# Kernel tuning notes

Hardware: AMD Instinct MI355X
Metric: run time of the kernel (lower is better)

## Reference

```python
import jax, jax.numpy as jnp
import numpy as np

N, E, IN, HID, H, L, G = 20000, 320000, 128, 64, 4, 3, 128

def setup_inputs() -> dict:
    key = jax.random.key(0)
    ks = jax.random.split(key, 14)
    x = jax.random.normal(ks[0], (N, IN), dtype=jnp.float32)
    edge_index = jax.random.randint(ks[1], (2, E), 0, N, dtype=jnp.int64)
    batch = jnp.sort(jax.random.randint(ks[2], (N,), 0, G, dtype=jnp.int64))
    s_in = 1.0 / np.sqrt(IN)
    s_h = 1.0 / np.sqrt(HID)
    lin_W = jax.random.normal(ks[3], (IN, HID), jnp.float32) * s_in
    lin_b = jax.random.normal(ks[4], (HID,), jnp.float32) * 0.02
    Wq = jax.random.normal(ks[5], (L, HID, H * HID), jnp.float32) * s_h
    bq = jax.random.normal(ks[6], (L, H * HID), jnp.float32) * 0.02
    Wk = jax.random.normal(ks[7], (L, HID, H * HID), jnp.float32) * s_h
    bk = jax.random.normal(ks[8], (L, H * HID), jnp.float32) * 0.02
    Wv = jax.random.normal(ks[9], (L, HID, H * HID), jnp.float32) * s_h
    bv = jax.random.normal(ks[10], (L, H * HID), jnp.float32) * 0.02
    Ws = jax.random.normal(ks[11], (L, HID, HID), jnp.float32) * s_h
    bs = jax.random.normal(ks[12], (L, HID), jnp.float32) * 0.02
    return {"x": x, "edge_index": edge_index, "batch": batch,
            "lin_W": lin_W, "lin_b": lin_b, "Wq": Wq, "bq": bq,
            "Wk": Wk, "bk": bk, "Wv": Wv, "bv": bv, "Ws": Ws, "bs": bs}

def _transformer_conv(h, src, dst, Wq, bq, Wk, bk, Wv, bv, Ws, bs):
    # PyG TransformerConv(hid, hid, heads=H, concat=False), beta=False, root_weight=True
    n = h.shape[0]
    C = HID  # per-head dim
    q = (h @ Wq + bq).reshape(n, H, C)
    k = (h @ Wk + bk).reshape(n, H, C)
    v = (h @ Wv + bv).reshape(n, H, C)
    # per-edge attention logits: q_i . k_j / sqrt(C), i=dst (target), j=src
    alpha = jnp.einsum('ehc,ehc->eh', q[dst], k[src]) * (1.0 / np.sqrt(C))  # [E,H]
    # segment softmax over edges grouped by target node
    amax = jax.ops.segment_max(alpha, dst, num_segments=n)  # [N,H]
    amax = jnp.where(jnp.isfinite(amax), amax, 0.0)
    ex = jnp.exp(alpha - amax[dst])
    denom = jax.ops.segment_sum(ex, dst, num_segments=n)
    a = ex / jnp.maximum(denom[dst], 1e-16)  # [E,H]
    msg = a[:, :, None] * v[src]  # [E,H,C]
    agg = jax.ops.segment_sum(msg.reshape(-1, H * C), dst, num_segments=n)
    out = agg.reshape(n, H, C).mean(axis=1)  # concat=False -> head mean
    return out + h @ Ws + bs  # root/skip connection

def reference(x, edge_index, batch, lin_W, lin_b, Wq, bq, Wk, bk, Wv, bv, Ws, bs):
    src, dst = edge_index[0], edge_index[1]
    h = x @ lin_W + lin_b  # [N, HID]; dropout inactive in eval
    for l in range(L):
        h = jax.nn.relu(_transformer_conv(h, src, dst, Wq[l], bq[l], Wk[l], bk[l],
                                          Wv[l], bv[l], Ws[l], bs[l]))
    # global_add_pool: sum node features per graph
    return jax.ops.segment_sum(h, batch, num_segments=G)  # [G, HID]
```

## Files before the change

kernel.cpp:

```cpp
#include <hip/hip_runtime.h>
#include <math.h>

#define N_NODES 20000
#define N_EDGES 320000
#define DIM_IN 128
#define HID 64
#define HEADS 4
#define LAYERS 3
#define GRAPHS 128
#define HOP 68

typedef unsigned short ushort;
typedef ushort ushort8 __attribute__((ext_vector_type(8)));
typedef ushort ushort4v __attribute__((ext_vector_type(4)));
typedef short short8 __attribute__((ext_vector_type(8)));
typedef float f32x4 __attribute__((ext_vector_type(4)));

__device__ __forceinline__ float bf2f(ushort u) {
    return __uint_as_float(((unsigned int)u) << 16);
}
__device__ __forceinline__ ushort f2bf(float f) {
    unsigned int b = __float_as_uint(f);
    return (ushort)((b + 0x7FFFu + ((b >> 16) & 1u)) >> 16);
}


__global__ __launch_bounds__(256) void histwcvt_kernel(
        const int* __restrict__ dst, int* __restrict__ counts,
        const float* __restrict__ Wq, const float* __restrict__ bq,
        const float* __restrict__ Wk, const float* __restrict__ bk,
        const float* __restrict__ Wv, const float* __restrict__ bv,
        const float* __restrict__ Ws, const float* __restrict__ bs,
        const float* __restrict__ linW,
        ushort* __restrict__ Wt3, float* __restrict__ bias3,
        ushort* __restrict__ Wlt) {
    const int PER = 832 * 64;
    int idx = blockIdx.x * 256 + threadIdx.x;
    if (idx < N_EDGES) atomicAdd(&counts[dst[idx]], 1);
    if (idx < 3 * PER) {
        int l = idx / PER;
        int r = idx - l * PER;
        int j = r >> 6, k = r & 63;
        const float* Wq_l = Wq + (size_t)l * HID * 256;
        const float* Wk_l = Wk + (size_t)l * HID * 256;
        const float* Wv_l = Wv + (size_t)l * HID * 256;
        const float* Ws_l = Ws + (size_t)l * HID * 64;
        float w;
        if (j < 256) {
            w = Wq_l[(size_t)k * 256 + j];
        } else if (j < 768) {
            int pout = j - 256;
            int isv = (pout >> 2) & 1;
            int low2 = pout & 3;
            int g = pout >> 3;
            int srccol = (g >> 4) * 64 + (g & 15) * 4 + low2;
            w = isv ? Wv_l[(size_t)k * 256 + srccol] : Wk_l[(size_t)k * 256 + srccol];
        } else {
            w = Ws_l[(size_t)k * 64 + (j - 768)];
        }
        Wt3[idx] = f2bf(w);
    } else if (idx < 3 * PER + 64 * DIM_IN) {
        int idx2 = idx - 3 * PER;
        int col = idx2 >> 7, k = idx2 & 127;
        Wlt[idx2] = f2bf(linW[(size_t)k * HID + col]);
    }
    if (idx < 3 * 832) {
        int l = idx / 832, j = idx - l * 832;
        float b;
        if (j < 256) {
            b = bq[l * 256 + j];
        } else if (j < 768) {
            int pout = j - 256;
            int isv = (pout >> 2) & 1;
            int low2 = pout & 3;
            int g = pout >> 3;
            int srccol = (g >> 4) * 64 + (g & 15) * 4 + low2;
            b = isv ? bv[l * 256 + srccol] : bk[l * 256 + srccol];
        } else {
            b = bs[l * 64 + (j - 768)];
        }
        bias3[idx] = b;
    }
}


__global__ __launch_bounds__(256) void blocksum_sortcnt_kernel(const int* __restrict__ counts,
        int* __restrict__ bsum, int* __restrict__ degcnt, int* __restrict__ rankbuf) {
    int i = blockIdx.x * 256 + threadIdx.x;
    int v = (i < N_NODES) ? counts[i] : 0;
    if (i < N_NODES) {
        int key = 1023 - (v < 1023 ? v : 1023);
        rankbuf[i] = atomicAdd(&degcnt[key], 1);
    }
    int lane = threadIdx.x & 63, wave = threadIdx.x >> 6;
    int s = v;
#pragma unroll
    for (int off = 32; off >= 1; off >>= 1) s += __shfl_xor(s, off);
    __shared__ int ws[4];
    if (lane == 0) ws[wave] = s;
    __syncthreads();
    if (threadIdx.x == 0) bsum[blockIdx.x] = ws[0] + ws[1] + ws[2] + ws[3];
}


__global__ __launch_bounds__(1024) void scans_kernel(const int* __restrict__ degcnt,
        int* __restrict__ degoff, const int* __restrict__ bsum, int* __restrict__ bexcl,
        int nb) {
    int tid = threadIdx.x;
    int v = degcnt[tid];
    int lane = tid & 63, wv = tid >> 6;
    int s = v;
#pragma unroll
    for (int off = 1; off < 64; off <<= 1) {
        int t = __shfl_up(s, off);
        if (lane >= off) s += t;
    }
    __shared__ int wsum[16];
    if (lane == 63) wsum[wv] = s;
    __syncthreads();
    int add = 0;
    for (int q = 0; q < wv; ++q) add += wsum[q];
    degoff[tid] = add + s - v;
    if (tid < 64) {
        int v0 = (tid < nb) ? bsum[tid] : 0;
        int s0 = v0;
#pragma unroll
        for (int off = 1; off < 64; off <<= 1) {
            int t = __shfl_up(s0, off);
            if (lane >= off) s0 += t;
        }
        int carry = __shfl(s0, 63);
        int v1 = (tid + 64 < nb) ? bsum[tid + 64] : 0;
        int s1 = v1;
#pragma unroll
        for (int off = 1; off < 64; off <<= 1) {
            int t = __shfl_up(s1, off);
            if (lane >= off) s1 += t;
        }
        if (tid < nb) bexcl[tid] = s0 - v0;
        if (tid + 64 < nb) bexcl[tid + 64] = carry + s1 - v1;
    }
}


__global__ __launch_bounds__(256) void expand_sortscat_kernel(const int* __restrict__ counts,
        const int* __restrict__ bexcl, int* __restrict__ offs, int* __restrict__ cursor,
        const int* __restrict__ degoff, const int* __restrict__ rankbuf,
        int* __restrict__ perm) {
    int i = blockIdx.x * 256 + threadIdx.x;
    int v = (i < N_NODES) ? counts[i] : 0;
    int lane = threadIdx.x & 63, wave = threadIdx.x >> 6;
    int s = v;
#pragma unroll
    for (int off = 1; off < 64; off <<= 1) {
        int t = __shfl_up(s, off);
        if (lane >= off) s += t;
    }
    __shared__ int wsum[4];
    if (lane == 63) wsum[wave] = s;
    __syncthreads();
    int add = bexcl[blockIdx.x];
    for (int w = 0; w < wave; ++w) add += wsum[w];
    int excl = add + s - v;
    if (i < N_NODES) {
        offs[i] = excl;
        cursor[i] = excl;
        int key = 1023 - (v < 1023 ? v : 1023);
        perm[degoff[key] + rankbuf[i]] = i;
    }
    if (i == 0) offs[N_NODES] = N_EDGES;
}

__global__ void scatter_kernel(const int* __restrict__ src, const int* __restrict__ dst,
                               int* __restrict__ cursor, int* __restrict__ csr, int n) {
    int e = blockIdx.x * 256 + threadIdx.x;
    if (e < n) {
        int d = dst[e];
        int pos = atomicAdd(&cursor[d], 1);
        csr[pos] = src[e];
    }
}


__device__ __forceinline__ void proj_rows(const float* __restrict__ ho,
        const ushort* __restrict__ Wt, const float* __restrict__ bias_cat,
        ushort* __restrict__ qsb, ushort* __restrict__ kvp,
        int grow, bool ok, int lane, int t0, int tstep) {
    int lr = lane & 15;
    int koff = (lane >> 4) * 8;
    short8 bh[2];
#pragma unroll
    for (int mm = 0; mm < 2; ++mm) {
        const float* hp = ho + lr * HOP + mm * 32 + koff;
        float4 f0 = *(const float4*)hp;
        float4 f1 = *(const float4*)(hp + 4);
        ushort8 u;
        u[0] = f2bf(f0.x); u[1] = f2bf(f0.y); u[2] = f2bf(f0.z); u[3] = f2bf(f0.w);
        u[4] = f2bf(f1.x); u[5] = f2bf(f1.y); u[6] = f2bf(f1.z); u[7] = f2bf(f1.w);
        bh[mm] = __builtin_bit_cast(short8, u);
    }
    for (int t = t0; t < 52; t += tstep) {
        const ushort* wb = Wt + (size_t)(t * 16 + lr) * HID + koff;
        short8 w0 = *(const short8*)wb;
        short8 w1 = *(const short8*)(wb + 32);
        f32x4 a_ = (f32x4){0.f, 0.f, 0.f, 0.f};
        a_ = __builtin_amdgcn_mfma_f32_16x16x32_bf16(w0, bh[0], a_, 0, 0, 0);
        a_ = __builtin_amdgcn_mfma_f32_16x16x32_bf16(w1, bh[1], a_, 0, 0, 0);
        int j = t * 16 + ((lane >> 4) << 2);
        float4 bs4 = *(const float4*)(bias_cat + j);
        ushort4v u4;
        u4[0] = f2bf(a_[0] + bs4.x);
        u4[1] = f2bf(a_[1] + bs4.y);
        u4[2] = f2bf(a_[2] + bs4.z);
        u4[3] = f2bf(a_[3] + bs4.w);
        if (ok) {
            ushort* dst;
            if (j < 256)      dst = qsb + (size_t)grow * 320 + j;
            else if (j < 768) dst = kvp + (size_t)grow * 512 + (j - 256);
            else              dst = qsb + (size_t)grow * 320 + 256 + (j - 768);
            *(ushort4v*)dst = u4;
        }
    }
}


__global__ __launch_bounds__(256) void linproj_kernel(const float* __restrict__ x,
        const ushort* __restrict__ Wlt, const float* __restrict__ lb,
        const ushort* __restrict__ Wt0, const float* __restrict__ bias0,
        ushort* __restrict__ qsb, ushort* __restrict__ kvp) {
    __shared__ float ho[64 * HOP];
    int tid = threadIdx.x;
    int w = tid >> 6, l = tid & 63;
    int r0 = blockIdx.x * 64 + w * 16;
    int row = r0 + (l & 15);
    int rowc = (row < N_NODES) ? row : (N_NODES - 1);

    short8 a[4];
#pragma unroll
    for (int kc = 0; kc < 4; ++kc) {
        const float* xp = x + (size_t)rowc * DIM_IN + kc * 32 + (l >> 4) * 8;
        float4 f0 = *(const float4*)xp;
        float4 f1 = *(const float4*)(xp + 4);
        ushort8 u;
        u[0] = f2bf(f0.x); u[1] = f2bf(f0.y); u[2] = f2bf(f0.z); u[3] = f2bf(f0.w);
        u[4] = f2bf(f1.x); u[5] = f2bf(f1.y); u[6] = f2bf(f1.z); u[7] = f2bf(f1.w);
        a[kc] = __builtin_bit_cast(short8, u);
    }

    f32x4 acc[4];
#pragma unroll
    for (int t = 0; t < 4; ++t) acc[t] = (f32x4){0.f, 0.f, 0.f, 0.f};

    const ushort* wb = Wlt + (size_t)(l & 15) * DIM_IN + (l >> 4) * 8;
#pragma unroll
    for (int t = 0; t < 4; ++t) {
#pragma unroll
        for (int kc = 0; kc < 4; ++kc) {
            short8 b = *(const short8*)(wb + (size_t)t * 16 * DIM_IN + kc * 32);
            acc[t] = __builtin_amdgcn_mfma_f32_16x16x32_bf16(b, a[kc], acc[t], 0, 0, 0);
        }
    }

    float* hrow = ho + (size_t)(w * 16 + (l & 15)) * HOP;
#pragma unroll
    for (int t = 0; t < 4; ++t) {
        int j = t * 16 + ((l >> 4) << 2);
        float4 bias = *(const float4*)(lb + j);
        float4 o;
        o.x = acc[t][0] + bias.x;
        o.y = acc[t][1] + bias.y;
        o.z = acc[t][2] + bias.z;
        o.w = acc[t][3] + bias.w;
        *(float4*)(hrow + j) = o;
    }
    proj_rows(ho + (size_t)w * 16 * HOP, Wt0, bias0, qsb, kvp,
              row, row < N_NODES, l, 0, 1);
}


__device__ __forceinline__ float4 attn_node(int node, int lane,
        const ushort* __restrict__ qsb, const ushort8* __restrict__ kvp,
        const int* __restrict__ offs, const int* __restrict__ csr) {
    int hh = lane >> 4;
    int cb = (lane & 15) * 4;
    const ushort* nb = qsb + (size_t)node * 320;
    ushort4v qu = *(const ushort4v*)(nb + hh * 64 + cb);
    float qx = bf2f(qu[0]), qy = bf2f(qu[1]), qz = bf2f(qu[2]), qw = bf2f(qu[3]);

    const float SCL = 0.125f * 1.44269504088896340736f;
    float m = -INFINITY, l = 0.f;
    float4 acc = make_float4(0.f, 0.f, 0.f, 0.f);

    int e0 = offs[node], e1 = offs[node + 1];
    int cnt = e1 - e0;

    ushort8 cur = (ushort8)(0);
    ushort8 nxt = (ushort8)(0);
    if (cnt > 0) cur = kvp[(size_t)csr[e0] * 64 + lane];
    if (cnt > 1) nxt = kvp[(size_t)csr[e0 + 1] * 64 + lane];

    for (int i = 0; i < cnt; ++i) {
        ushort8 u = cur;
        cur = nxt;
        if (i + 2 < cnt) nxt = kvp[(size_t)csr[e0 + i + 2] * 64 + lane];

        float p = qx * bf2f(u[0]) + qy * bf2f(u[1]) + qz * bf2f(u[2]) + qw * bf2f(u[3]);
        p += __shfl_xor(p, 1);
        p += __shfl_xor(p, 2);
        p += __shfl_xor(p, 4);
        p += __shfl_xor(p, 8);
        float alpha = p * SCL;
        if (__any(alpha > m)) {
            float nm = fmaxf(m, alpha);
            float sc = exp2f(m - nm);
            l *= sc; acc.x *= sc; acc.y *= sc; acc.z *= sc; acc.w *= sc;
            m = nm;
        }
        float pe = exp2f(alpha - m);
        l += pe;
        acc.x += pe * bf2f(u[4]);
        acc.y += pe * bf2f(u[5]);
        acc.z += pe * bf2f(u[6]);
        acc.w += pe * bf2f(u[7]);
    }

    float inv = (l > 0.f) ? (1.f / l) : 0.f;
    float4 r;
    r.x = acc.x * inv;
    r.y = acc.y * inv;
    r.z = acc.z * inv;
    r.w = acc.w * inv;
    r.x += __shfl_xor(r.x, 16); r.x += __shfl_xor(r.x, 32);
    r.y += __shfl_xor(r.y, 16); r.y += __shfl_xor(r.y, 32);
    r.z += __shfl_xor(r.z, 16); r.z += __shfl_xor(r.z, 32);
    r.w += __shfl_xor(r.w, 16); r.w += __shfl_xor(r.w, 32);

    ushort4v su = *(const ushort4v*)(nb + 256 + cb);
    float4 o;
    o.x = fmaxf(r.x * 0.25f + bf2f(su[0]), 0.f);
    o.y = fmaxf(r.y * 0.25f + bf2f(su[1]), 0.f);
    o.z = fmaxf(r.z * 0.25f + bf2f(su[2]), 0.f);
    o.w = fmaxf(r.w * 0.25f + bf2f(su[3]), 0.f);
    return o;
}


__global__ __launch_bounds__(1024) void edgeproj_kernel(const ushort* __restrict__ qsb_in,
        const ushort8* __restrict__ kvp_in,
        const int* __restrict__ offs, const int* __restrict__ csr,
        const int* __restrict__ perm,
        const ushort* __restrict__ Wt_next, const float* __restrict__ bias_next,
        ushort* __restrict__ qsb_out, ushort* __restrict__ kvp_out) {
    __shared__ float ho[16 * HOP];
    int tid = threadIdx.x;
    int w = tid >> 6, l = tid & 63;
    int node = perm[blockIdx.x * 16 + w];
    float4 o = attn_node(node, l, qsb_in, kvp_in, offs, csr);
    if ((l >> 4) == 0)
        *(float4*)(ho + (size_t)w * HOP + (l & 15) * 4) = o;
    __syncthreads();
    int grow = perm[blockIdx.x * 16 + (l & 15)];
    proj_rows(ho, Wt_next, bias_next, qsb_out, kvp_out, grow, true, l, w, 16);
}


__global__ __launch_bounds__(256) void edgepool_kernel(const ushort* __restrict__ qsb,
        const ushort8* __restrict__ kvp,
        const int* __restrict__ offs, const int* __restrict__ csr,
        const int* __restrict__ batch, float* __restrict__ out) {
    int w = threadIdx.x >> 6, l = threadIdx.x & 63;
    int node = blockIdx.x * 4 + w;
    float4 o = attn_node(node, l, qsb, kvp, offs, csr);
    if ((l >> 4) == 0) {
        int g = batch[node];
        float* op = out + (size_t)g * HID + (l & 15) * 4;
        atomicAdd(op + 0, o.x);
        atomicAdd(op + 1, o.y);
        atomicAdd(op + 2, o.z);
        atomicAdd(op + 3, o.w);
    }
}


extern "C" void kernel_launch(void* const* d_in, const int* in_sizes, int n_in,
                              void* d_out, int out_size, void* d_ws, size_t ws_size,
                              hipStream_t stream) {
    const float* x    = (const float*)d_in[0];
    const int*   edge = (const int*)d_in[1];
    const int*   batch= (const int*)d_in[2];
    const float* linW = (const float*)d_in[3];
    const float* linb = (const float*)d_in[4];
    const float* Wq   = (const float*)d_in[5];
    const float* bq   = (const float*)d_in[6];
    const float* Wk   = (const float*)d_in[7];
    const float* bk   = (const float*)d_in[8];
    const float* Wv   = (const float*)d_in[9];
    const float* bv   = (const float*)d_in[10];
    const float* Ws   = (const float*)d_in[11];
    const float* bs   = (const float*)d_in[12];
    float* out = (float*)d_out;

    const int* src = edge;
    const int* dst = edge + N_EDGES;

    ushort* qsb0 = (ushort*)d_ws;
    ushort* qsb1 = qsb0 + (size_t)N_NODES * 320;
    ushort* kvp0 = qsb1 + (size_t)N_NODES * 320;
    ushort* kvp1 = kvp0 + (size_t)N_NODES * 512;
    int* counts = (int*)(kvp1 + (size_t)N_NODES * 512);
    int* degcnt = counts + N_NODES;
    int* offs   = degcnt + 1024;
    int* cursor = offs + N_NODES + 1;
    int* csr    = cursor + N_NODES;
    int* bsum   = csr + N_EDGES;
    int* bexcl  = bsum + 128;
    int* degoff = bexcl + 128;
    int* rankbuf= degoff + 1024;
    int* perm   = rankbuf + N_NODES;
    ushort* Wt3 = (ushort*)(perm + N_NODES);
    float* bias3 = (float*)(Wt3 + 3 * 832 * 64);
    ushort* Wlt = (ushort*)(bias3 + 3 * 832);

    const int NB = (N_NODES + 255) / 256;

    hipMemsetAsync(counts, 0, (N_NODES + 1024) * sizeof(int), stream);
    hipMemsetAsync(out, 0, (size_t)GRAPHS * HID * sizeof(float), stream);

    histwcvt_kernel<<<(N_EDGES + 255) / 256, 256, 0, stream>>>(
        dst, counts, Wq, bq, Wk, bk, Wv, bv, Ws, bs, linW, Wt3, bias3, Wlt);

    blocksum_sortcnt_kernel<<<NB, 256, 0, stream>>>(counts, bsum, degcnt, rankbuf);

    scans_kernel<<<1, 1024, 0, stream>>>(degcnt, degoff, bsum, bexcl, NB);

    expand_sortscat_kernel<<<NB, 256, 0, stream>>>(counts, bexcl, offs, cursor,
                                                   degoff, rankbuf, perm);

    scatter_kernel<<<(N_EDGES + 255) / 256, 256, 0, stream>>>(src, dst, cursor, csr, N_EDGES);

    linproj_kernel<<<(N_NODES + 63) / 64, 256, 0, stream>>>(
        x, Wlt, linb, Wt3, bias3, qsb0, kvp0);

    edgeproj_kernel<<<N_NODES / 16, 1024, 0, stream>>>(
        qsb0, (const ushort8*)kvp0, offs, csr, perm,
        Wt3 + (size_t)1 * 832 * 64, bias3 + 832, qsb1, kvp1);

    edgeproj_kernel<<<N_NODES / 16, 1024, 0, stream>>>(
        qsb1, (const ushort8*)kvp1, offs, csr, perm,
        Wt3 + (size_t)2 * 832 * 64, bias3 + 1664, qsb0, kvp0);

    edgepool_kernel<<<N_NODES / 4, 256, 0, stream>>>(
        qsb0, (const ushort8*)kvp0, offs, csr, batch, out);
}
```

Before: 443.5 us.

## Fuse CSR scatter into linear projection and replace atomic pooling with sorted segment reduction

The edge scatter that builds the CSR is merged into the first projection kernel, so one launch handles both: all blocks scatter edges and the first 313 blocks also run the projection. The final layer now writes per-node features to a buffer, and a separate pool kernel binary-searches the sorted batch array to sum each graph's rows, replacing per-node float atomics and the output memset. This removes one launch and atomic contention on the output, but adds a launch for pooling, an extra write and read of node features, and relies on batch being sorted.

```diff
diff --git a/kernel.cpp b/kernel.cpp
--- a/kernel.cpp
+++ b/kernel.cpp
@@ -9,6 +9,7 @@
 #define LAYERS 3
 #define GRAPHS 128
 #define HOP 68
+#define LINPROJ_BLOCKS 313
 
 typedef unsigned short ushort;
 typedef ushort ushort8 __attribute__((ext_vector_type(8)));
@@ -171,16 +172,6 @@
     if (i == 0) offs[N_NODES] = N_EDGES;
 }
 
-__global__ void scatter_kernel(const int* __restrict__ src, const int* __restrict__ dst,
-                               int* __restrict__ cursor, int* __restrict__ csr, int n) {
-    int e = blockIdx.x * 256 + threadIdx.x;
-    if (e < n) {
-        int d = dst[e];
-        int pos = atomicAdd(&cursor[d], 1);
-        csr[pos] = src[e];
-    }
-}
-
 
 __device__ __forceinline__ void proj_rows(const float* __restrict__ ho,
         const ushort* __restrict__ Wt, const float* __restrict__ bias_cat,
@@ -224,10 +215,20 @@
 }
 
 
-__global__ __launch_bounds__(256) void linproj_kernel(const float* __restrict__ x,
+__global__ __launch_bounds__(256) void linprojscat_kernel(const float* __restrict__ x,
         const ushort* __restrict__ Wlt, const float* __restrict__ lb,
         const ushort* __restrict__ Wt0, const float* __restrict__ bias0,
-        ushort* __restrict__ qsb, ushort* __restrict__ kvp) {
+        ushort* __restrict__ qsb, ushort* __restrict__ kvp,
+        const int* __restrict__ src, const int* __restrict__ dst,
+        int* __restrict__ cursor, int* __restrict__ csr) {
+    int e = blockIdx.x * 256 + threadIdx.x;
+    if (e < N_EDGES) {
+        int d = dst[e];
+        int pos = atomicAdd(&cursor[d], 1);
+        csr[pos] = src[e];
+    }
+    if (blockIdx.x >= LINPROJ_BLOCKS) return;
+
     __shared__ float ho[64 * HOP];
     int tid = threadIdx.x;
     int w = tid >> 6, l = tid & 63;
@@ -364,21 +365,36 @@
 }
 
 
-__global__ __launch_bounds__(256) void edgepool_kernel(const ushort* __restrict__ qsb,
+__global__ __launch_bounds__(256) void edge_kernel(const ushort* __restrict__ qsb,
         const ushort8* __restrict__ kvp,
         const int* __restrict__ offs, const int* __restrict__ csr,
-        const int* __restrict__ batch, float* __restrict__ out) {
+        float* __restrict__ hout) {
     int w = threadIdx.x >> 6, l = threadIdx.x & 63;
     int node = blockIdx.x * 4 + w;
     float4 o = attn_node(node, l, qsb, kvp, offs, csr);
-    if ((l >> 4) == 0) {
-        int g = batch[node];
-        float* op = out + (size_t)g * HID + (l & 15) * 4;
-        atomicAdd(op + 0, o.x);
-        atomicAdd(op + 1, o.y);
-        atomicAdd(op + 2, o.z);
-        atomicAdd(op + 3, o.w);
-    }
+    if ((l >> 4) == 0)
+        *(float4*)(hout + (size_t)node * HID + (l & 15) * 4) = o;
+}
+
+
+__global__ __launch_bounds__(256) void pool_kernel(const float* __restrict__ h,
+                                                   const int* __restrict__ batch,
+                                                   float* __restrict__ out) {
+    int g = blockIdx.x;
+    int lo = 0, hi = N_NODES;
+    while (lo < hi) { int mid = (lo + hi) >> 1; if (batch[mid] < g) lo = mid + 1; else hi = mid; }
+    int start = lo;
+    hi = N_NODES;
+    while (lo < hi) { int mid = (lo + hi) >> 1; if (batch[mid] < g + 1) lo = mid + 1; else hi = mid; }
+    int end = lo;
+    int c = threadIdx.x & 63;
+    int sub = threadIdx.x >> 6;
+    float acc = 0.f;
+    for (int i = start + sub; i < end; i += 4) acc += h[(size_t)i * HID + c];
+    __shared__ float lds[4][64];
+    lds[sub][c] = acc;
+    __syncthreads();
+    if (sub == 0) out[g * HID + c] = lds[0][c] + lds[1][c] + lds[2][c] + lds[3][c];
 }
 
 
@@ -407,6 +423,7 @@
     ushort* qsb1 = qsb0 + (size_t)N_NODES * 320;
     ushort* kvp0 = qsb1 + (size_t)N_NODES * 320;
     ushort* kvp1 = kvp0 + (size_t)N_NODES * 512;
+    float*  h3   = (float*)kvp1;
     int* counts = (int*)(kvp1 + (size_t)N_NODES * 512);
     int* degcnt = counts + N_NODES;
     int* offs   = degcnt + 1024;
@@ -424,7 +441,6 @@
     const int NB = (N_NODES + 255) / 256;
 
     hipMemsetAsync(counts, 0, (N_NODES + 1024) * sizeof(int), stream);
-    hipMemsetAsync(out, 0, (size_t)GRAPHS * HID * sizeof(float), stream);
 
     histwcvt_kernel<<<(N_EDGES + 255) / 256, 256, 0, stream>>>(
         dst, counts, Wq, bq, Wk, bk, Wv, bv, Ws, bs, linW, Wt3, bias3, Wlt);
@@ -436,10 +452,8 @@
     expand_sortscat_kernel<<<NB, 256, 0, stream>>>(counts, bexcl, offs, cursor,
                                                    degoff, rankbuf, perm);
 
-    scatter_kernel<<<(N_EDGES + 255) / 256, 256, 0, stream>>>(src, dst, cursor, csr, N_EDGES);
-
-    linproj_kernel<<<(N_NODES + 63) / 64, 256, 0, stream>>>(
-        x, Wlt, linb, Wt3, bias3, qsb0, kvp0);
+    linprojscat_kernel<<<(N_EDGES + 255) / 256, 256, 0, stream>>>(
+        x, Wlt, linb, Wt3, bias3, qsb0, kvp0, src, dst, cursor, csr);
 
     edgeproj_kernel<<<N_NODES / 16, 1024, 0, stream>>>(
         qsb0, (const ushort8*)kvp0, offs, csr, perm,
@@ -449,6 +463,8 @@
         qsb1, (const ushort8*)kvp1, offs, csr, perm,
         Wt3 + (size_t)2 * 832 * 64, bias3 + 1664, qsb0, kvp0);
 
-    edgepool_kernel<<<N_NODES / 4, 256, 0, stream>>>(
-        qsb0, (const ushort8*)kvp0, offs, csr, batch, out);
-}
+    edge_kernel<<<N_NODES / 4, 256, 0, stream>>>(
+        qsb0, (const ushort8*)kvp0, offs, csr, h3);
+
+    pool_kernel<<<GRAPHS, 256, 0, stream>>>(h3, batch, out);
+}
```

Result: faster. 424.5 us (-4.3%).
